# Performance work log

Measured on AMD Instinct MI355X. Metric: run time of the kernel, lower is better.

The kernel has to match this reference:

```python
import jax, jax.numpy as jnp
import numpy as np

N, E, T, F, H, OUT, HORIZON = 50000, 1600000, 12, 16, 128, 3, 6
TARGET_IDX = (0, 1, 2)


def setup_inputs() -> dict:
    key = jax.random.key(0)
    ks = jax.random.split(key, 20)
    inp = {
        'x_seq': jax.random.normal(ks[0], (T, N, F), jnp.float32),
        'ei_seq': jax.random.randint(ks[1], (T, 2, E), 0, N, jnp.int32),
        'ea_seq': jax.random.uniform(ks[2], (T, E), jnp.float32),
        'mask_seq': jax.random.bernoulli(ks[3], 0.9, (T, N)),
    }
    sF = 1.0 / np.sqrt(F)
    s2H = 1.0 / np.sqrt(2 * H)
    sH = 1.0 / np.sqrt(H)
    # GCNConv weights (x @ W, W: [F,H]) + biases for z, r, h gates
    for i, g in enumerate(['z', 'r', 'h']):
        inp['Wc' + g] = jax.random.normal(ks[4 + i], (F, H), jnp.float32) * sF
        inp['bc' + g] = jnp.zeros((H,), jnp.float32)
        # Linear(2H, H) stored as [2H, H] for x @ W
        inp['Wl' + g] = jax.random.normal(ks[8 + i], (2 * H, H), jnp.float32) * s2H
        inp['bl' + g] = jnp.zeros((H,), jnp.float32)
    inp['head_W'] = jax.random.normal(ks[12], (H, OUT), jnp.float32) * sH
    inp['head_b'] = jnp.zeros((OUT,), jnp.float32)
    return inp


def _gcn(x, src, dst, ew, W, b):
    # GCNConv with self-loops and symmetric normalization
    loop = jnp.arange(N, dtype=src.dtype)
    s = jnp.concatenate([src, loop])
    d = jnp.concatenate([dst, loop])
    w = jnp.concatenate([ew, jnp.ones((N,), ew.dtype)])
    deg = jax.ops.segment_sum(w, d, num_segments=N)
    dinv = jnp.where(deg > 0, jax.lax.rsqrt(jnp.maximum(deg, 1e-12)), 0.0)
    norm = dinv[s] * w * dinv[d]                      # [E+N]
    xw = x @ W                                        # [N,H]
    return jax.ops.segment_sum(norm[:, None] * xw[s], d, num_segments=N) + b


def _tgcn_cell(x, ei, ew, h, p):
    src, dst = ei[0], ei[1]
    z = jax.nn.sigmoid(
        jnp.concatenate([_gcn(x, src, dst, ew, p['Wcz'], p['bcz']), h], axis=1) @ p['Wlz'] + p['blz'])
    r = jax.nn.sigmoid(
        jnp.concatenate([_gcn(x, src, dst, ew, p['Wcr'], p['bcr']), h], axis=1) @ p['Wlr'] + p['blr'])
    h_tilde = jnp.tanh(
        jnp.concatenate([_gcn(x, src, dst, ew, p['Wch'], p['bch']), h * r], axis=1) @ p['Wlh'] + p['blh'])
    return z * h + (1.0 - z) * h_tilde


def reference(x_seq, ei_seq, ea_seq, mask_seq,
              Wcz, bcz, Wlz, blz, Wcr, bcr, Wlr, blr, Wch, bch, Wlh, blh,
              head_W, head_b):
    p = dict(Wcz=Wcz, bcz=bcz, Wlz=Wlz, blz=blz, Wcr=Wcr, bcr=bcr,
             Wlr=Wlr, blr=blr, Wch=Wch, bch=bch, Wlh=Wlh, blh=blh)

    def step(carry, inputs):
        h_state, seen = carry
        x, ei, ew, m = inputs
        # h_dict lookup: only nodes present now AND seen before carry state
        h_prev = jnp.where((m & seen)[:, None], h_state, 0.0)
        h_new = _tgcn_cell(x, ei, ew, h_prev, p)
        h_state = jnp.where(m[:, None], h_new, h_state)   # h_dict scatter update
        return (h_state, seen | m), None

    init = (jnp.zeros((N, H), x_seq.dtype), jnp.zeros((N,), bool))
    (h_state, _), _ = jax.lax.scan(step, init, (x_seq, ei_seq, ea_seq, mask_seq))

    # final gather: nodes present at last step are all in h_dict after the loop
    h_prev = jnp.where(mask_seq[-1][:, None], h_state, 0.0)
    x_last, ei_last, ew_last = x_seq[-1], ei_seq[-1], ea_seq[-1]
    ti = jnp.array(TARGET_IDX)
    preds = []
    for _ in range(HORIZON):
        inp = x_last if not preds else x_last.at[:, ti].set(preds[-1])
        h_new = _tgcn_cell(inp, ei_last, ew_last, h_prev, p)
        preds.append(h_new @ head_W + head_b)   # dropout is identity in eval
        h_prev = h_new
    return jnp.stack(preds, axis=0)             # [HORIZON, N, OUT]
```

## Files before the change

kernel.cpp:

```cpp
#include <hip/hip_runtime.h>
#include <math.h>

#define NN 50000
#define TT 12
#define EE 1600000
#define FF 16
#define HH 128
#define CHK 4096
#define NCH 391
#define BKT 128
#define NBINS 391
#define CAP 6144
#define RP 50016
#define CGB 782
#define AR_STR 136
#define AX_STR 40
#define HC_STR 136
#define BKROW 160

typedef _Float16 half8_t __attribute__((ext_vector_type(8)));
typedef float floatx4 __attribute__((ext_vector_type(4)));

__device__ __forceinline__ float h16_to_f(unsigned short u) {
    _Float16 h; __builtin_memcpy(&h, &u, 2); return (float)h;
}
__device__ __forceinline__ unsigned short f_to_h16(float f) {
    _Float16 h = (_Float16)f; unsigned short u; __builtin_memcpy(&u, &h, 2); return u;
}
__device__ __forceinline__ float fsig(float x) {
    return 1.0f / (1.0f + exp2f(-1.44269504f * x));
}
__device__ __forceinline__ float ftanh(float x) {
    return 2.0f / (1.0f + exp2f(-2.88539009f * x)) - 1.0f;
}

__global__ void detect_mask(const unsigned char* __restrict__ m, int* __restrict__ flag) {
    __shared__ int cnt[2];
    if (threadIdx.x < 2) cnt[threadIdx.x] = 0;
    __syncthreads();
    int a = 0, b = 0;
    for (int base = 0; base < 4096; base += 256) {
        int idx = base + threadIdx.x;
        unsigned char v = m[idx];
        int r = idx & 3;
        if (v) { if (r == 0) a++; else if (r == 1) b++; }
    }
    atomicAdd(&cnt[0], a);
    atomicAdd(&cnt[1], b);
    __syncthreads();
    if (threadIdx.x == 0) flag[0] = cnt[1] > 0 ? 0 : (cnt[0] > 0 ? 1 : 2);
}

__global__ void build_masks(const void* __restrict__ mask, const int* __restrict__ flag,
                            unsigned char* __restrict__ hm, unsigned char* __restrict__ mc) {
    int n = blockIdx.x * 256 + threadIdx.x;
    if (n >= NN) return;
    int mode = flag[0];
    bool seen = false;
    for (int t = 0; t < TT; t++) {
        int idx = t * NN + n;
        bool m;
        if (mode == 0)      m = ((const unsigned char*)mask)[idx] != 0;
        else if (mode == 1) m = ((const int*)mask)[idx] != 0;
        else                m = ((const float*)mask)[idx] != 0.0f;
        hm[idx] = (m && seen) ? 1 : 0;
        mc[idx] = m ? 1 : 0;
        seen = seen || m;
    }
}

__global__ void hist_kernel(const int* __restrict__ ei, int* __restrict__ chunkHist) {
    __shared__ int h[NBINS + 1];
    int c = blockIdx.x, t = blockIdx.y, tid = threadIdx.x;
    for (int i = tid; i < NBINS; i += 256) h[i] = 0;
    __syncthreads();
    const int* dstp = ei + (size_t)(2 * t + 1) * EE;
    int e0 = c * CHK;
    for (int i = tid; i < CHK; i += 256) {
        int e = e0 + i;
        if (e < EE) atomicAdd(&h[dstp[e] >> 7], 1);
    }
    __syncthreads();
    for (int i = tid; i < NBINS; i += 256)
        chunkHist[((size_t)t * NBINS + i) * NCH + c] = h[i];
}

__global__ void scan_kernel(int* __restrict__ buf) {
    __shared__ int ps[1024];
    const int L = NBINS * NCH;
    const int PER = 150;
    int t = blockIdx.x, tid = threadIdx.x;
    int* a = buf + (size_t)t * L;
    int i0 = tid * PER, i1 = min(i0 + PER, L);
    int s = 0;
    for (int i = i0; i < i1; i++) s += a[i];
    ps[tid] = s;
    __syncthreads();
    for (int off = 1; off < 1024; off <<= 1) {
        int v = (tid >= off) ? ps[tid - off] : 0;
        __syncthreads();
        ps[tid] += v;
        __syncthreads();
    }
    int base = (tid == 0) ? 0 : ps[tid - 1];
    for (int i = i0; i < i1; i++) { int v = a[i]; a[i] = base; base += v; }
}

__launch_bounds__(256)
__global__ void scatter_kernel(const int* __restrict__ ei, const float* __restrict__ ea,
                               const int* __restrict__ chunkOff, uint2* __restrict__ E2,
                               int batch) {
    __shared__ uint2 sorted[CHK];
    __shared__ int cnt[NBINS];
    __shared__ int sA[NBINS], sB[NBINS];
    __shared__ int start[NBINS], gbase[NBINS];
    int c = blockIdx.x, y = blockIdx.y, tid = threadIdx.x;
    int t = batch * 6 + y;
    for (int i = tid; i < NBINS; i += 256) {
        cnt[i] = 0;
        gbase[i] = chunkOff[((size_t)t * NBINS + i) * NCH + c];
    }
    __syncthreads();
    const int* srcp = ei + (size_t)(2 * t) * EE;
    const int* dstp = ei + (size_t)(2 * t + 1) * EE;
    const float* wp = ea + (size_t)t * EE;
    int e0 = c * CHK;
    int m = min(CHK, EE - e0);
    uint2 rec[16];
    int rank[16];
#pragma unroll
    for (int k = 0; k < 16; k++) {
        int i = k * 256 + tid;
        rank[k] = -1;
        if (i < m) {
            int e = e0 + i;
            unsigned int s = (unsigned int)srcp[e];
            unsigned int d = (unsigned int)dstp[e];
            float wv = wp[e];
            rec[k].x = s | (d << 16);
            rec[k].y = __float_as_uint(wv);
            rank[k] = atomicAdd(&cnt[d >> 7], 1);
        }
    }
    __syncthreads();
    for (int i = tid; i < NBINS; i += 256) sA[i] = cnt[i];
    __syncthreads();
    int pp = 0;
    for (int off = 1; off < NBINS; off <<= 1) {
        if (pp == 0) {
            for (int i = tid; i < NBINS; i += 256)
                sB[i] = (i >= off) ? sA[i] + sA[i - off] : sA[i];
        } else {
            for (int i = tid; i < NBINS; i += 256)
                sA[i] = (i >= off) ? sB[i] + sB[i - off] : sB[i];
        }
        pp ^= 1;
        __syncthreads();
    }
    const int* inc = pp ? sB : sA;
    for (int i = tid; i < NBINS; i += 256) start[i] = inc[i] - cnt[i];
    __syncthreads();
#pragma unroll
    for (int k = 0; k < 16; k++) {
        if (rank[k] >= 0) {
            int b = rec[k].x >> 23;
            sorted[start[b] + rank[k]] = rec[k];
        }
    }
    __syncthreads();
    uint2* outp = E2 + (size_t)y * EE;
    for (int i = tid; i < m; i += 256) {
        uint2 r = sorted[i];
        int b = r.x >> 23;
        outp[gbase[b] + (i - start[b])] = r;
    }
}

__launch_bounds__(256)
__global__ void sortbin_kernel(const uint2* __restrict__ E2, const int* __restrict__ chunkHist,
                               unsigned int* __restrict__ E1, int* __restrict__ rowptr,
                               float* __restrict__ dinvG, int batch) {
    __shared__ uint2 es[CAP];
    __shared__ int cnt[BKT];
    __shared__ float wsm[BKT];
    __shared__ int cur[BKT];
    int b = blockIdx.x, y = blockIdx.y, tid = threadIdx.x;
    int t = batch * 6 + y;
    const uint2* gE = E2 + (size_t)y * EE;
    unsigned int* oE = E1 + (size_t)t * EE;
    const int* off = chunkHist + (size_t)t * NBINS * NCH;
    int e0 = off[b * NCH];
    int e1 = (b == NBINS - 1) ? EE : off[(b + 1) * NCH];
    int seg = e1 - e0;
    for (int i = tid; i < seg; i += 256) es[i] = gE[e0 + i];
    if (tid < BKT) { cnt[tid] = 0; wsm[tid] = 0.0f; }
    __syncthreads();
    for (int i = tid; i < seg; i += 256) {
        int dl = (es[i].x >> 16) & 127;
        atomicAdd(&cnt[dl], 1);
        atomicAdd(&wsm[dl], __uint_as_float(es[i].y));
    }
    __syncthreads();
    int ogv = (tid < BKT) ? cnt[tid] : 0;
    for (int o = 1; o < BKT; o <<= 1) {
        int u = (tid < BKT && tid >= o) ? cnt[tid - o] : 0;
        __syncthreads();
        if (tid < BKT) cnt[tid] += u;
        __syncthreads();
    }
    if (tid < BKT) {
        int exc = cnt[tid] - ogv;
        cur[tid] = exc;
        float dv = rsqrtf(1.0f + wsm[tid]);
        wsm[tid] = dv;
        int node = b * BKT + tid;
        if (node <= NN) {
            rowptr[(size_t)t * RP + node] = e0 + exc;
            if (node < NN) dinvG[(size_t)t * NN + node] = dv;
        }
    }
    __syncthreads();
    for (int i = tid; i < seg; i += 256) {
        uint2 p = es[i];
        int dl = (p.x >> 16) & 127;
        int pos = atomicAdd(&cur[dl], 1);
        float wv = __uint_as_float(p.y) * wsm[dl];
        oE[e0 + pos] = (p.x & 0xFFFF) | ((unsigned int)f_to_h16(wv) << 16);
    }
}

__global__ void xs_kernel(const float* __restrict__ x, const float* __restrict__ dinvG,
                          _Float16* __restrict__ xs16) {
    int gid = blockIdx.x * 256 + threadIdx.x;
    int tn = gid >> 2;
    float dd = dinvG[tn];
    float4 v = ((const float4*)x)[gid];
    _Float16 h[4] = {(_Float16)(dd * v.x), (_Float16)(dd * v.y),
                     (_Float16)(dd * v.z), (_Float16)(dd * v.w)};
    uint2 o;
    __builtin_memcpy(&o, h, 8);
    ((uint2*)xs16)[gid] = o;
}

__global__ void gather_csr(const unsigned int* __restrict__ E1, const int* __restrict__ rowptr,
                           const float* __restrict__ dinvG, const _Float16* __restrict__ xs16,
                           _Float16* __restrict__ xagg16) {
    int t = blockIdx.y;
    int n = blockIdx.x * 4 + (threadIdx.x >> 6);
    if (n >= NN) return;
    int lane = threadIdx.x & 63;
    int eo = lane >> 3, fp = lane & 7;
    const unsigned int* gE = E1 + (size_t)t * EE;
    const _Float16* xs = xs16 + (size_t)t * NN * FF;
    int r0 = rowptr[(size_t)t * RP + n], r1 = rowptr[(size_t)t * RP + n + 1];
    float a0 = 0.0f, a1 = 0.0f;
    int e = r0 + eo;
    for (; e + 8 < r1; e += 16) {
        unsigned int recA = gE[e];
        unsigned int recB = gE[e + 8];
        unsigned int xpA = *(const unsigned int*)(xs + (size_t)(recA & 0xFFFF) * FF + 2 * fp);
        unsigned int xpB = *(const unsigned int*)(xs + (size_t)(recB & 0xFFFF) * FF + 2 * fp);
        float wA = h16_to_f((unsigned short)(recA >> 16));
        float wB = h16_to_f((unsigned short)(recB >> 16));
        a0 += wA * h16_to_f((unsigned short)(xpA & 0xFFFF));
        a1 += wA * h16_to_f((unsigned short)(xpA >> 16));
        a0 += wB * h16_to_f((unsigned short)(xpB & 0xFFFF));
        a1 += wB * h16_to_f((unsigned short)(xpB >> 16));
    }
    if (e < r1) {
        unsigned int rec = gE[e];
        float wv = h16_to_f((unsigned short)(rec >> 16));
        unsigned int xp = *(const unsigned int*)(xs + (size_t)(rec & 0xFFFF) * FF + 2 * fp);
        a0 += wv * h16_to_f((unsigned short)(xp & 0xFFFF));
        a1 += wv * h16_to_f((unsigned short)(xp >> 16));
    }
    a0 += __shfl_xor(a0, 8);  a1 += __shfl_xor(a1, 8);
    a0 += __shfl_xor(a0, 16); a1 += __shfl_xor(a1, 16);
    a0 += __shfl_xor(a0, 32); a1 += __shfl_xor(a1, 32);
    if (eo == 0) {
        float dd = dinvG[(size_t)t * NN + n];
        unsigned int xp = *(const unsigned int*)(xs + (size_t)n * FF + 2 * fp);
        float o0 = a0 + dd * h16_to_f((unsigned short)(xp & 0xFFFF));
        float o1 = a1 + dd * h16_to_f((unsigned short)(xp >> 16));
        unsigned int pack = (unsigned int)f_to_h16(o0) | ((unsigned int)f_to_h16(o1) << 16);
        ((unsigned int*)(xagg16 + ((size_t)t * NN + n) * FF))[fp] = pack;
    }
}

__global__ void gather3_csr(const unsigned int* __restrict__ E1, const int* __restrict__ rowptr,
                            const float* __restrict__ dinvG, const float* __restrict__ predsc,
                            _Float16* __restrict__ xaggH16) {
    int n = blockIdx.x * 4 + (threadIdx.x >> 6);
    if (n >= NN) return;
    int lane = threadIdx.x & 63;
    int eo = lane >> 2, f = lane & 3;
    const unsigned int* gE = E1 + (size_t)11 * EE;
    const float* dv = dinvG + (size_t)11 * NN;
    int r0 = rowptr[(size_t)11 * RP + n], r1 = rowptr[(size_t)11 * RP + n + 1];
    float acc = 0.0f;
    int e = r0 + eo;
    for (; e + 16 < r1; e += 32) {
        unsigned int recA = gE[e];
        unsigned int recB = gE[e + 16];
        if (f < 3) {
            float pA = predsc[(size_t)(recA & 0xFFFF) * 4 + f];
            float pB = predsc[(size_t)(recB & 0xFFFF) * 4 + f];
            acc += h16_to_f((unsigned short)(recA >> 16)) * pA;
            acc += h16_to_f((unsigned short)(recB >> 16)) * pB;
        }
    }
    if (e < r1) {
        unsigned int rec = gE[e];
        if (f < 3)
            acc += h16_to_f((unsigned short)(rec >> 16)) * predsc[(size_t)(rec & 0xFFFF) * 4 + f];
    }
    acc += __shfl_xor(acc, 4);
    acc += __shfl_xor(acc, 8);
    acc += __shfl_xor(acc, 16);
    acc += __shfl_xor(acc, 32);
    if (lane < 3) {
        float res = acc + dv[n] * predsc[(size_t)n * 4 + f];
        xaggH16[(size_t)n * FF + f] = (_Float16)res;
    }
}

__global__ void weight_kernel(const float* Wc0, const float* bc0, const float* Wl0, const float* bl0,
                              const float* Wc1, const float* bc1, const float* Wl1, const float* bl1,
                              const float* Wc2, const float* bc2, const float* Wl2, const float* bl2,
                              _Float16* __restrict__ BcatT, float* __restrict__ beff) {
    __shared__ float WcS[FF][HH];
    int g = blockIdx.x;
    int n = threadIdx.x;
    const float* Wc = g == 0 ? Wc0 : (g == 1 ? Wc1 : Wc2);
    const float* bc = g == 0 ? bc0 : (g == 1 ? bc1 : bc2);
    const float* Wl = g == 0 ? Wl0 : (g == 1 ? Wl1 : Wl2);
    const float* bl = g == 0 ? bl0 : (g == 1 ? bl1 : bl2);
    for (int q = 0; q < FF; q++) WcS[q][n] = Wc[q * HH + n];
    __syncthreads();
    float acc[FF];
#pragma unroll
    for (int i = 0; i < FF; i++) acc[i] = 0.0f;
    float accb = 0.0f;
    for (int k = 0; k < HH; k++) {
        float wl = Wl[k * HH + n];
        accb += bc[k] * wl;
#pragma unroll
        for (int i = 0; i < FF; i++) acc[i] += WcS[i][k] * wl;
    }
    _Float16* row = BcatT + ((size_t)g * HH + n) * BKROW;
    for (int j = 0; j < HH; j++) row[j] = (_Float16)Wl[(size_t)(HH + j) * HH + n];
#pragma unroll
    for (int i = 0; i < FF; i++) row[HH + i] = (_Float16)acc[i];
#pragma unroll
    for (int i = 144; i < 160; i++) row[i] = (_Float16)0.0f;
    beff[g * HH + n] = bl[n] + accb;
}

__launch_bounds__(512, 2)
__global__ void cellseq_kernel(const _Float16* __restrict__ xaggBase,
                               _Float16* __restrict__ hio,
                               const _Float16* __restrict__ BcatT,
                               const float* __restrict__ beff,
                               const unsigned char* __restrict__ hmAll,
                               const unsigned char* __restrict__ mcAll,
                               int nsteps) {
    __shared__ _Float16 Hc[64 * HC_STR];
    __shared__ _Float16 Ar[64 * AR_STR];
    __shared__ _Float16 Ax[64 * AX_STR];
    const int tid = threadIdx.x;
    const int m0 = blockIdx.x * 64;
    const int lane = tid & 63;
    const int w = tid >> 6;
    const int mrow = lane & 15;
    const int quad = lane >> 4;
    const int col0 = w * 16;
    const int cb = col0 + quad * 4;
    const bool rec = (hmAll != nullptr);

    const float4 bz4 = *(const float4*)(beff + cb);
    const float4 br4 = *(const float4*)(beff + HH + cb);
    const float4 bh4 = *(const float4*)(beff + 2 * HH + cb);

    const _Float16* Wzp = BcatT + (size_t)(col0 + mrow) * BKROW + quad * 8;
    half8_t wz[5], wr[5], wh[5];
#pragma unroll
    for (int ks = 0; ks < 5; ks++) {
        wz[ks] = *(const half8_t*)(Wzp + ks * 32);
        wr[ks] = *(const half8_t*)(Wzp + (size_t)HH * BKROW + ks * 32);
        wh[ks] = *(const half8_t*)(Wzp + (size_t)2 * HH * BKROW + ks * 32);
    }

    for (int idx = tid; idx < 128; idx += 512) {
        int row = idx >> 1, q = idx & 1;
        *(uint4*)(Ax + row * AX_STR + 16 + q * 8) = make_uint4(0, 0, 0, 0);
    }
    for (int idx = tid; idx < 1024; idx += 512) {
        int row = idx >> 4, q = idx & 15;
        int g = m0 + row;
        uint4 v = make_uint4(0, 0, 0, 0);
        if (!rec && g < NN) v = *(const uint4*)(hio + (size_t)g * HH + q * 8);
        *(uint4*)(Hc + row * HC_STR + q * 8) = v;
    }
    __syncthreads();

    const half8_t h8z = {0, 0, 0, 0, 0, 0, 0, 0};

    for (int t = 0; t < nsteps; t++) {
        const _Float16* xa = xaggBase + (size_t)t * NN * FF;
        const unsigned char* hm = rec ? (hmAll + (size_t)t * NN) : nullptr;
        const unsigned char* mc = rec ? (mcAll + (size_t)t * NN) : nullptr;

        for (int idx = tid; idx < 128; idx += 512) {
            int row = idx >> 1, q = idx & 1;
            int g = m0 + row;
            uint4 v = make_uint4(0, 0, 0, 0);
            if (g < NN) v = *(const uint4*)(xa + (size_t)g * FF + q * 8);
            *(uint4*)(Ax + row * AX_STR + q * 8) = v;
        }
        __syncthreads();

        floatx4 zacc[4];
        unsigned int hpw[4][2];
#pragma unroll
        for (int nt = 0; nt < 4; nt++) {
            int node = nt * 16 + mrow;
            int g = m0 + node;
            bool m = (g < NN) && (!rec || hm[g] != 0);
            const _Float16* hp = Hc + node * HC_STR;
            half8_t hx[5];
#pragma unroll
            for (int ks = 0; ks < 4; ks++) {
                half8_t v = *(const half8_t*)(hp + ks * 32 + quad * 8);
                hx[ks] = m ? v : h8z;
            }
            hx[4] = *(const half8_t*)(Ax + node * AX_STR + quad * 8);
            floatx4 za = {0.0f, 0.0f, 0.0f, 0.0f}, ra = {0.0f, 0.0f, 0.0f, 0.0f};
#pragma unroll
            for (int ks = 0; ks < 5; ks++)
                za = __builtin_amdgcn_mfma_f32_16x16x32_f16(wz[ks], hx[ks], za, 0, 0, 0);
#pragma unroll
            for (int ks = 0; ks < 5; ks++)
                ra = __builtin_amdgcn_mfma_f32_16x16x32_f16(wr[ks], hx[ks], ra, 0, 0, 0);
            zacc[nt] = za;
            uint2 hpr = *(const uint2*)(hp + cb);
            uint2 hpv = m ? hpr : make_uint2(0, 0);
            hpw[nt][0] = hpv.x; hpw[nt][1] = hpv.y;
            float r0 = fsig(ra[0] + br4.x), r1 = fsig(ra[1] + br4.y);
            float r2 = fsig(ra[2] + br4.z), r3 = fsig(ra[3] + br4.w);
            float hp0 = h16_to_f((unsigned short)(hpv.x & 0xFFFF));
            float hp1 = h16_to_f((unsigned short)(hpv.x >> 16));
            float hp2 = h16_to_f((unsigned short)(hpv.y & 0xFFFF));
            float hp3 = h16_to_f((unsigned short)(hpv.y >> 16));
            uint2 o;
            o.x = (unsigned int)f_to_h16(hp0 * r0) | ((unsigned int)f_to_h16(hp1 * r1) << 16);
            o.y = (unsigned int)f_to_h16(hp2 * r2) | ((unsigned int)f_to_h16(hp3 * r3) << 16);
            *(uint2*)(Ar + node * AR_STR + cb) = o;
        }
        __syncthreads();

#pragma unroll
        for (int nt = 0; nt < 4; nt++) {
            int node = nt * 16 + mrow;
            const _Float16* ap = Ar + node * AR_STR;
            half8_t hx[5];
#pragma unroll
            for (int ks = 0; ks < 4; ks++) hx[ks] = *(const half8_t*)(ap + ks * 32 + quad * 8);
            hx[4] = *(const half8_t*)(Ax + node * AX_STR + quad * 8);
            floatx4 ha = {0.0f, 0.0f, 0.0f, 0.0f};
#pragma unroll
            for (int ks = 0; ks < 5; ks++)
                ha = __builtin_amdgcn_mfma_f32_16x16x32_f16(wh[ks], hx[ks], ha, 0, 0, 0);
            int g = m0 + node;
            if (g < NN) {
                float z0 = fsig(zacc[nt][0] + bz4.x), z1 = fsig(zacc[nt][1] + bz4.y);
                float z2 = fsig(zacc[nt][2] + bz4.z), z3 = fsig(zacc[nt][3] + bz4.w);
                float t0 = ftanh(ha[0] + bh4.x), t1 = ftanh(ha[1] + bh4.y);
                float t2 = ftanh(ha[2] + bh4.z), t3 = ftanh(ha[3] + bh4.w);
                float hp0 = h16_to_f((unsigned short)(hpw[nt][0] & 0xFFFF));
                float hp1 = h16_to_f((unsigned short)(hpw[nt][0] >> 16));
                float hp2 = h16_to_f((unsigned short)(hpw[nt][1] & 0xFFFF));
                float hp3 = h16_to_f((unsigned short)(hpw[nt][1] >> 16));
                float n0 = z0 * hp0 + (1.0f - z0) * t0;
                float n1 = z1 * hp1 + (1.0f - z1) * t1;
                float n2 = z2 * hp2 + (1.0f - z2) * t2;
                float n3 = z3 * hp3 + (1.0f - z3) * t3;
                uint2 o;
                o.x = (unsigned int)f_to_h16(n0) | ((unsigned int)f_to_h16(n1) << 16);
                o.y = (unsigned int)f_to_h16(n2) | ((unsigned int)f_to_h16(n3) << 16);
                if (rec) {
                    if (mc[g]) *(uint2*)(Hc + node * HC_STR + cb) = o;
                } else {
                    *(uint2*)(hio + (size_t)g * HH + cb) = o;
                }
            }
        }
        __syncthreads();
    }

    if (rec) {
        const unsigned char* mcL = mcAll + (size_t)(nsteps - 1) * NN;
        for (int idx = tid; idx < 1024; idx += 512) {
            int row = idx >> 4, q = idx & 15;
            int g = m0 + row;
            if (g < NN) {
                uint4 v = make_uint4(0, 0, 0, 0);
                if (mcL[g]) v = *(const uint4*)(Hc + row * HC_STR + q * 8);
                *(uint4*)(hio + (size_t)g * HH + q * 8) = v;
            }
        }
    }
}

__global__ void head_kernel(const _Float16* __restrict__ hp, const float* __restrict__ headW,
                            const float* __restrict__ headb, const float* __restrict__ dinv11,
                            float* __restrict__ out, float* __restrict__ predsc) {
    int node = (blockIdx.x * 256 + threadIdx.x) >> 6;
    int lane = threadIdx.x & 63;
    if (node >= NN) return;
    const _Float16* h = hp + (size_t)node * HH;
    float h0 = (float)h[lane], h1 = (float)h[64 + lane];
    float s0 = h0 * headW[lane * 3 + 0] + h1 * headW[(64 + lane) * 3 + 0];
    float s1 = h0 * headW[lane * 3 + 1] + h1 * headW[(64 + lane) * 3 + 1];
    float s2 = h0 * headW[lane * 3 + 2] + h1 * headW[(64 + lane) * 3 + 2];
#pragma unroll
    for (int off = 32; off > 0; off >>= 1) {
        s0 += __shfl_down(s0, off);
        s1 += __shfl_down(s1, off);
        s2 += __shfl_down(s2, off);
    }
    if (lane == 0) {
        float o0 = s0 + headb[0], o1 = s1 + headb[1], o2 = s2 + headb[2];
        out[(size_t)node * 3 + 0] = o0;
        out[(size_t)node * 3 + 1] = o1;
        out[(size_t)node * 3 + 2] = o2;
        float dd = dinv11[node];
        predsc[(size_t)node * 4 + 0] = dd * o0;
        predsc[(size_t)node * 4 + 1] = dd * o1;
        predsc[(size_t)node * 4 + 2] = dd * o2;
    }
}

extern "C" void kernel_launch(void* const* d_in, const int* in_sizes, int n_in,
                              void* d_out, int out_size, void* d_ws, size_t ws_size,
                              hipStream_t stream) {
    const float* x = (const float*)d_in[0];
    const int* ei = (const int*)d_in[1];
    const float* ea = (const float*)d_in[2];
    const void* mask = d_in[3];
    const float* Wc[3] = {(const float*)d_in[4], (const float*)d_in[8], (const float*)d_in[12]};
    const float* bc[3] = {(const float*)d_in[5], (const float*)d_in[9], (const float*)d_in[13]};
    const float* Wl[3] = {(const float*)d_in[6], (const float*)d_in[10], (const float*)d_in[14]};
    const float* bl[3] = {(const float*)d_in[7], (const float*)d_in[11], (const float*)d_in[15]};
    const float* headW = (const float*)d_in[16];
    const float* headb = (const float*)d_in[17];
    float* out = (float*)d_out;

    char* w = (char*)d_ws;
    auto alloc = [&](size_t bytes) {
        char* p = w;
        w += (bytes + 255) & ~(size_t)255;
        return p;
    };
    float* dinv = (float*)alloc((size_t)TT * NN * 4);
    _Float16* xagg16 = (_Float16*)alloc((size_t)TT * NN * FF * 2);
    _Float16* xaggH16 = (_Float16*)alloc((size_t)NN * FF * 2);
    _Float16* xs16 = (_Float16*)alloc((size_t)TT * NN * FF * 2);
    int* chunkHist = (int*)alloc((size_t)TT * NBINS * NCH * 4);
    int* rowptr = (int*)alloc((size_t)TT * RP * 4);
    unsigned int* E1 = (unsigned int*)alloc((size_t)TT * EE * 4);
    uint2* E2 = (uint2*)alloc((size_t)6 * EE * 8);
    _Float16* BcatT = (_Float16*)alloc((size_t)3 * HH * BKROW * 2);
    float* beff = (float*)alloc(3 * HH * 4);
    float* predsc = (float*)alloc((size_t)NN * 4 * 4);
    unsigned char* hm = (unsigned char*)alloc((size_t)TT * NN);
    unsigned char* mc = (unsigned char*)alloc((size_t)TT * NN);
    int* flag = (int*)alloc(64);

    _Float16* hph = (_Float16*)E2;

    detect_mask<<<1, 256, 0, stream>>>((const unsigned char*)mask, flag);
    build_masks<<<(NN + 255) / 256, 256, 0, stream>>>(mask, flag, hm, mc);

    hist_kernel<<<dim3(NCH, TT), 256, 0, stream>>>(ei, chunkHist);
    scan_kernel<<<TT, 1024, 0, stream>>>(chunkHist);
    for (int b = 0; b < 2; b++) {
        scatter_kernel<<<dim3(NCH, 6), 256, 0, stream>>>(ei, ea, chunkHist, E2, b);
        sortbin_kernel<<<dim3(NBINS, 6), 256, 0, stream>>>(E2, chunkHist, E1, rowptr, dinv, b);
    }
    xs_kernel<<<TT * NN * 4 / 256, 256, 0, stream>>>(x, dinv, xs16);
    gather_csr<<<dim3((NN + 3) / 4, TT), 256, 0, stream>>>(E1, rowptr, dinv, xs16, xagg16);

    weight_kernel<<<3, 128, 0, stream>>>(Wc[0], bc[0], Wl[0], bl[0],
                                         Wc[1], bc[1], Wl[1], bl[1],
                                         Wc[2], bc[2], Wl[2], bl[2], BcatT, beff);

    cellseq_kernel<<<CGB, 512, 0, stream>>>(xagg16, hph, BcatT, beff, hm, mc, TT);

    hipMemcpyAsync(xaggH16, xagg16 + (size_t)11 * NN * FF, (size_t)NN * FF * 2,
                   hipMemcpyDeviceToDevice, stream);

    for (int k = 0; k < 6; k++) {
        const _Float16* xa = (k == 0) ? (xagg16 + (size_t)11 * NN * FF) : xaggH16;
        cellseq_kernel<<<CGB, 512, 0, stream>>>(xa, hph, BcatT, beff, nullptr, nullptr, 1);
        head_kernel<<<NN * 64 / 256, 256, 0, stream>>>(hph, headW, headb, dinv + (size_t)11 * NN,
                                                       out + (size_t)k * NN * 3, predsc);
        if (k < 5) {
            gather3_csr<<<(NN + 3) / 4, 256, 0, stream>>>(E1, rowptr, dinv, predsc, xaggH16);
        }
    }
}
```

Before: 1.916 ms.

## Double-buffer hidden state and x-aggregate in LDS, keep recurrent state in registers

Double-buffers the hidden-state and x-aggregate LDS tiles so the next step's x-aggregate is prefetched while the current step's h-gate MFMAs run. The hidden state is kept per-thread in registers, and the masked input for the next step is written into the alternate buffer. This removes one __syncthreads and the load phase at the top of each step, folds the per-element mask selects into a single write, and drops the final copy-out loop. The cost is more LDS (a second H and Ax buffer) and more registers, which could reduce occupancy at 512 threads with launch_bounds of 2 blocks.

Measured after the change: 1.881 ms. Within noise of the previous version (-1.9%).

```diff
diff --git a/kernel.cpp b/kernel.cpp
--- a/kernel.cpp
+++ b/kernel.cpp
@@ -13,9 +13,9 @@
 #define CAP 6144
 #define RP 50016
 #define CGB 782
+#define H_STR 136
 #define AR_STR 136
 #define AX_STR 40
-#define HC_STR 136
 #define BKROW 160
 
 typedef _Float16 half8_t __attribute__((ext_vector_type(8)));
@@ -364,9 +364,9 @@
                                const unsigned char* __restrict__ hmAll,
                                const unsigned char* __restrict__ mcAll,
                                int nsteps) {
-    __shared__ _Float16 Hc[64 * HC_STR];
+    __shared__ _Float16 Hin[2][64 * H_STR];
     __shared__ _Float16 Ar[64 * AR_STR];
-    __shared__ _Float16 Ax[64 * AX_STR];
+    __shared__ _Float16 Ax[2][64 * AX_STR];
     const int tid = threadIdx.x;
     const int m0 = blockIdx.x * 64;
     const int lane = tid & 63;
@@ -390,50 +390,45 @@
         wh[ks] = *(const half8_t*)(Wzp + (size_t)2 * HH * BKROW + ks * 32);
     }
 
+    for (int idx = tid; idx < 256; idx += 512) {
+        int buf = idx >> 7, r2 = idx & 127;
+        int row = r2 >> 1, q = r2 & 1;
+        *(uint4*)(Ax[buf] + row * AX_STR + 16 + q * 8) = make_uint4(0, 0, 0, 0);
+    }
     for (int idx = tid; idx < 128; idx += 512) {
         int row = idx >> 1, q = idx & 1;
-        *(uint4*)(Ax + row * AX_STR + 16 + q * 8) = make_uint4(0, 0, 0, 0);
+        int g = m0 + row;
+        uint4 v = make_uint4(0, 0, 0, 0);
+        if (g < NN) v = *(const uint4*)(xaggBase + (size_t)g * FF + q * 8);
+        *(uint4*)(Ax[0] + row * AX_STR + q * 8) = v;
     }
     for (int idx = tid; idx < 1024; idx += 512) {
         int row = idx >> 4, q = idx & 15;
         int g = m0 + row;
         uint4 v = make_uint4(0, 0, 0, 0);
         if (!rec && g < NN) v = *(const uint4*)(hio + (size_t)g * HH + q * 8);
-        *(uint4*)(Hc + row * HC_STR + q * 8) = v;
-    }
-    __syncthreads();
-
-    const half8_t h8z = {0, 0, 0, 0, 0, 0, 0, 0};
-
+        *(uint4*)(Hin[0] + row * H_STR + q * 8) = v;
+    }
+    uint2 hreg[4];
+#pragma unroll
+    for (int nt = 0; nt < 4; nt++) hreg[nt] = make_uint2(0, 0);
+    __syncthreads();
+
+    int cur = 0;
     for (int t = 0; t < nsteps; t++) {
-        const _Float16* xa = xaggBase + (size_t)t * NN * FF;
-        const unsigned char* hm = rec ? (hmAll + (size_t)t * NN) : nullptr;
-        const unsigned char* mc = rec ? (mcAll + (size_t)t * NN) : nullptr;
-
-        for (int idx = tid; idx < 128; idx += 512) {
-            int row = idx >> 1, q = idx & 1;
-            int g = m0 + row;
-            uint4 v = make_uint4(0, 0, 0, 0);
-            if (g < NN) v = *(const uint4*)(xa + (size_t)g * FF + q * 8);
-            *(uint4*)(Ax + row * AX_STR + q * 8) = v;
-        }
-        __syncthreads();
+        const _Float16* Hc = Hin[cur];
+        const _Float16* Axc = Ax[cur];
 
         floatx4 zacc[4];
-        unsigned int hpw[4][2];
+        uint2 hpv[4];
 #pragma unroll
         for (int nt = 0; nt < 4; nt++) {
             int node = nt * 16 + mrow;
-            int g = m0 + node;
-            bool m = (g < NN) && (!rec || hm[g] != 0);
-            const _Float16* hp = Hc + node * HC_STR;
+            const _Float16* hp = Hc + node * H_STR;
             half8_t hx[5];
 #pragma unroll
-            for (int ks = 0; ks < 4; ks++) {
-                half8_t v = *(const half8_t*)(hp + ks * 32 + quad * 8);
-                hx[ks] = m ? v : h8z;
-            }
-            hx[4] = *(const half8_t*)(Ax + node * AX_STR + quad * 8);
+            for (int ks = 0; ks < 4; ks++) hx[ks] = *(const half8_t*)(hp + ks * 32 + quad * 8);
+            hx[4] = *(const half8_t*)(Axc + node * AX_STR + quad * 8);
             floatx4 za = {0.0f, 0.0f, 0.0f, 0.0f}, ra = {0.0f, 0.0f, 0.0f, 0.0f};
 #pragma unroll
             for (int ks = 0; ks < 5; ks++)
@@ -442,22 +437,39 @@
             for (int ks = 0; ks < 5; ks++)
                 ra = __builtin_amdgcn_mfma_f32_16x16x32_f16(wr[ks], hx[ks], ra, 0, 0, 0);
             zacc[nt] = za;
-            uint2 hpr = *(const uint2*)(hp + cb);
-            uint2 hpv = m ? hpr : make_uint2(0, 0);
-            hpw[nt][0] = hpv.x; hpw[nt][1] = hpv.y;
+            uint2 hp2 = *(const uint2*)(hp + cb);
+            hpv[nt] = hp2;
             float r0 = fsig(ra[0] + br4.x), r1 = fsig(ra[1] + br4.y);
             float r2 = fsig(ra[2] + br4.z), r3 = fsig(ra[3] + br4.w);
-            float hp0 = h16_to_f((unsigned short)(hpv.x & 0xFFFF));
-            float hp1 = h16_to_f((unsigned short)(hpv.x >> 16));
-            float hp2 = h16_to_f((unsigned short)(hpv.y & 0xFFFF));
-            float hp3 = h16_to_f((unsigned short)(hpv.y >> 16));
+            float hp0 = h16_to_f((unsigned short)(hp2.x & 0xFFFF));
+            float hp1 = h16_to_f((unsigned short)(hp2.x >> 16));
+            float hp2f = h16_to_f((unsigned short)(hp2.y & 0xFFFF));
+            float hp3 = h16_to_f((unsigned short)(hp2.y >> 16));
             uint2 o;
             o.x = (unsigned int)f_to_h16(hp0 * r0) | ((unsigned int)f_to_h16(hp1 * r1) << 16);
-            o.y = (unsigned int)f_to_h16(hp2 * r2) | ((unsigned int)f_to_h16(hp3 * r3) << 16);
+            o.y = (unsigned int)f_to_h16(hp2f * r2) | ((unsigned int)f_to_h16(hp3 * r3) << 16);
             *(uint2*)(Ar + node * AR_STR + cb) = o;
         }
         __syncthreads();
 
+        const bool hasNext = (t + 1 < nsteps);
+        uint4 axn = make_uint4(0, 0, 0, 0);
+        if (hasNext && tid < 128) {
+            int row = tid >> 1, q = tid & 1;
+            int g = m0 + row;
+            if (g < NN)
+                axn = *(const uint4*)(xaggBase + (size_t)(t + 1) * NN * FF + (size_t)g * FF + q * 8);
+        }
+        bool mcb[4], hmb[4];
+#pragma unroll
+        for (int nt = 0; nt < 4; nt++) {
+            int g = m0 + nt * 16 + mrow;
+            mcb[nt] = false; hmb[nt] = false;
+            if (rec && g < NN) {
+                mcb[nt] = mcAll[(size_t)t * NN + g] != 0;
+                if (hasNext) hmb[nt] = hmAll[(size_t)(t + 1) * NN + g] != 0;
+            }
+        }
 #pragma unroll
         for (int nt = 0; nt < 4; nt++) {
             int node = nt * 16 + mrow;
@@ -465,49 +477,46 @@
             half8_t hx[5];
 #pragma unroll
             for (int ks = 0; ks < 4; ks++) hx[ks] = *(const half8_t*)(ap + ks * 32 + quad * 8);
-            hx[4] = *(const half8_t*)(Ax + node * AX_STR + quad * 8);
+            hx[4] = *(const half8_t*)(Axc + node * AX_STR + quad * 8);
             floatx4 ha = {0.0f, 0.0f, 0.0f, 0.0f};
 #pragma unroll
             for (int ks = 0; ks < 5; ks++)
                 ha = __builtin_amdgcn_mfma_f32_16x16x32_f16(wh[ks], hx[ks], ha, 0, 0, 0);
             int g = m0 + node;
-            if (g < NN) {
-                float z0 = fsig(zacc[nt][0] + bz4.x), z1 = fsig(zacc[nt][1] + bz4.y);
-                float z2 = fsig(zacc[nt][2] + bz4.z), z3 = fsig(zacc[nt][3] + bz4.w);
-                float t0 = ftanh(ha[0] + bh4.x), t1 = ftanh(ha[1] + bh4.y);
-                float t2 = ftanh(ha[2] + bh4.z), t3 = ftanh(ha[3] + bh4.w);
-                float hp0 = h16_to_f((unsigned short)(hpw[nt][0] & 0xFFFF));
-                float hp1 = h16_to_f((unsigned short)(hpw[nt][0] >> 16));
-                float hp2 = h16_to_f((unsigned short)(hpw[nt][1] & 0xFFFF));
-                float hp3 = h16_to_f((unsigned short)(hpw[nt][1] >> 16));
-                float n0 = z0 * hp0 + (1.0f - z0) * t0;
-                float n1 = z1 * hp1 + (1.0f - z1) * t1;
-                float n2 = z2 * hp2 + (1.0f - z2) * t2;
-                float n3 = z3 * hp3 + (1.0f - z3) * t3;
-                uint2 o;
-                o.x = (unsigned int)f_to_h16(n0) | ((unsigned int)f_to_h16(n1) << 16);
-                o.y = (unsigned int)f_to_h16(n2) | ((unsigned int)f_to_h16(n3) << 16);
-                if (rec) {
-                    if (mc[g]) *(uint2*)(Hc + node * HC_STR + cb) = o;
-                } else {
-                    *(uint2*)(hio + (size_t)g * HH + cb) = o;
+            float z0 = fsig(zacc[nt][0] + bz4.x), z1 = fsig(zacc[nt][1] + bz4.y);
+            float z2 = fsig(zacc[nt][2] + bz4.z), z3 = fsig(zacc[nt][3] + bz4.w);
+            float t0 = ftanh(ha[0] + bh4.x), t1 = ftanh(ha[1] + bh4.y);
+            float t2 = ftanh(ha[2] + bh4.z), t3 = ftanh(ha[3] + bh4.w);
+            float hp0 = h16_to_f((unsigned short)(hpv[nt].x & 0xFFFF));
+            float hp1 = h16_to_f((unsigned short)(hpv[nt].x >> 16));
+            float hp2 = h16_to_f((unsigned short)(hpv[nt].y & 0xFFFF));
+            float hp3 = h16_to_f((unsigned short)(hpv[nt].y >> 16));
+            float n0 = z0 * hp0 + (1.0f - z0) * t0;
+            float n1 = z1 * hp1 + (1.0f - z1) * t1;
+            float n2 = z2 * hp2 + (1.0f - z2) * t2;
+            float n3 = z3 * hp3 + (1.0f - z3) * t3;
+            uint2 o;
+            o.x = (unsigned int)f_to_h16(n0) | ((unsigned int)f_to_h16(n1) << 16);
+            o.y = (unsigned int)f_to_h16(n2) | ((unsigned int)f_to_h16(n3) << 16);
+            if (rec) {
+                if (mcb[nt]) hreg[nt] = o;
+                uint2 wv = (hasNext && hmb[nt]) ? hreg[nt] : make_uint2(0, 0);
+                if (hasNext) {
+                    *(uint2*)(Hin[cur ^ 1] + node * H_STR + cb) = wv;
+                } else if (g < NN) {
+                    uint2 fv = mcb[nt] ? hreg[nt] : make_uint2(0, 0);
+                    *(uint2*)(hio + (size_t)g * HH + cb) = fv;
                 }
+            } else if (g < NN) {
+                *(uint2*)(hio + (size_t)g * HH + cb) = o;
             }
         }
+        if (hasNext && tid < 128) {
+            int row = tid >> 1, q = tid & 1;
+            *(uint4*)(Ax[cur ^ 1] + row * AX_STR + q * 8) = axn;
+        }
         __syncthreads();
-    }
-
-    if (rec) {
-        const unsigned char* mcL = mcAll + (size_t)(nsteps - 1) * NN;
-        for (int idx = tid; idx < 1024; idx += 512) {
-            int row = idx >> 4, q = idx & 15;
-            int g = m0 + row;
-            if (g < NN) {
-                uint4 v = make_uint4(0, 0, 0, 0);
-                if (mcL[g]) v = *(const uint4*)(Hc + row * HC_STR + q * 8);
-                *(uint4*)(hio + (size_t)g * HH + q * 8) = v;
-            }
-        }
+        cur ^= 1;
     }
 }
 
```
